# Optimization experiments

Hardware: AMD Instinct MI355X
Metric: run time of the kernel (lower is better)

## Reference

```python
import jax, jax.numpy as jnp
import numpy as np

MARGIN = 0.3
N_GALLERY = 32768
N_BATCH = 1024
D_EMB = 512
N_CLASSES = 1000


def setup_inputs() -> dict:
    key = jax.random.key(0)
    k1, k2, k3, k4 = jax.random.split(key, 4)
    inputs = jax.random.normal(k1, (N_BATCH, D_EMB), dtype=jnp.float32)
    features = jax.random.normal(k2, (N_GALLERY, D_EMB), dtype=jnp.float32)
    feat_labels = jax.random.randint(k3, (N_GALLERY,), 0, N_CLASSES, dtype=jnp.int64 if jax.config.read('jax_enable_x64') else jnp.int32)
    idx = jax.random.randint(k4, (N_BATCH,), 0, N_GALLERY, dtype=feat_labels.dtype)
    # invariant from the original code: idx[i] is in the positive set for targets[i]
    targets = feat_labels[idx]
    return {"inputs": inputs, "features": features, "targets": targets,
            "idx": idx, "feat_labels": feat_labels}


def reference(inputs, features, targets, idx, feat_labels):
    # sim_mat: [n, N] similarity against the gallery bank
    sim = jnp.einsum('nd,Nd->nN', inputs, features)
    n = targets.shape[0]
    # positives: same label in gallery, excluding the sample's own gallery slot
    pos_mask = targets[:, None] == feat_labels[None, :]          # [n, N]
    pos_mask = pos_mask.at[jnp.arange(n), idx].set(False)
    # negatives: every gallery entry with a different label
    neg_mask = targets[:, None] != feat_labels[None, :]          # [n, N]
    pos = jnp.min(jnp.where(pos_mask, sim, jnp.inf), axis=1)     # hardest positive (lowest sim)
    neg = jnp.max(jnp.where(neg_mask, sim, -jnp.inf), axis=1)    # hardest negative (highest sim)
    loss = jnp.maximum(neg - pos + MARGIN, 0.0)
    return jnp.mean(loss)
```

## Files before the change

### kernel.cpp

```cpp
#include <hip/hip_runtime.h>
#include <stdint.h>

#define MARGIN 0.3f
#define M 1024
#define NG 32768
#define K 512
#define BM 256
#define BN 256
#define BK 64
#define KT (K / BK)
#define NTILES (NG / BN)
#define MTILES (M / BM)
#define NPART (NTILES * 4)

typedef __attribute__((ext_vector_type(8))) __bf16 bf16x8;
typedef __attribute__((ext_vector_type(4))) float f32x4;
typedef unsigned short ushort_t;
typedef unsigned int uint_t;

#define BAR() __builtin_amdgcn_s_barrier()
#define LGKM0() asm volatile("s_waitcnt lgkmcnt(0)" ::: "memory")
#define SGB0() __builtin_amdgcn_sched_barrier(0)

static __device__ __forceinline__ ushort_t f2bf(float f) {
    uint_t u = __float_as_uint(f);
    u += 0x7FFFu + ((u >> 16) & 1u);
    return (ushort_t)(u >> 16);
}

__global__ __launch_bounds__(256) void cvt_kernel(const float* __restrict__ src,
                                                  ushort_t* __restrict__ dst, int n8) {
    int i = blockIdx.x * 256 + threadIdx.x;
    if (i >= n8) return;
    const float4* s4 = (const float4*)src;
    float4 a = s4[2 * i];
    float4 b = s4[2 * i + 1];
    uint4 o;
    o.x = (uint_t)f2bf(a.x) | ((uint_t)f2bf(a.y) << 16);
    o.y = (uint_t)f2bf(a.z) | ((uint_t)f2bf(a.w) << 16);
    o.z = (uint_t)f2bf(b.x) | ((uint_t)f2bf(b.y) << 16);
    o.w = (uint_t)f2bf(b.z) | ((uint_t)f2bf(b.w) << 16);
    ((uint4*)dst)[i] = o;
}

static __device__ __forceinline__ void gload_lds16(const void* gptr, void* lptr) {
    __builtin_amdgcn_global_load_lds(
        (const __attribute__((address_space(1))) uint32_t*)(gptr),
        (__attribute__((address_space(3))) uint32_t*)(uintptr_t)(lptr),
        16, 0, 0);
}

static __device__ __forceinline__ bf16x8 lds_read_b128(const ushort_t* p) {
    bf16x8 r;
    asm volatile("ds_read_b128 %0, %1"
                 : "=v"(r)
                 : "v"((const __attribute__((address_space(3))) ushort_t*)p));
    return r;
}

__global__ __launch_bounds__(512, 2) void gemm_kernel(
    const ushort_t* __restrict__ A,
    const ushort_t* __restrict__ B,
    const int* __restrict__ targets,
    const int* __restrict__ idxv,
    const int* __restrict__ labels,
    float* __restrict__ pos_part,
    float* __restrict__ neg_part) {

    __shared__ __align__(16) ushort_t sA[2][BM * BK];
    __shared__ __align__(16) ushort_t sB[2][BN * BK];
    __shared__ int t_s[BM];
    __shared__ int i_s[BM];
    __shared__ int l_s[BN];

    const int tid = threadIdx.x;
    const int lane = tid & 63;
    const int w = tid >> 6;
    const int wm = w >> 2;
    const int wn = w & 3;
    const int l15 = lane & 15;
    const int lhi = lane >> 4;
    const int bid = blockIdx.x;
    const int ntile = bid & (NTILES - 1);
    const int mtile = bid >> 7;

    if (tid < BM) {
        t_s[tid] = targets[mtile * BM + tid];
        i_s[tid] = idxv[mtile * BM + tid];
    } else {
        l_s[tid - BM] = labels[ntile * BN + (tid - BM)];
    }

    f32x4 zero = {0.f, 0.f, 0.f, 0.f};
    f32x4 acc[8][4];
#pragma unroll
    for (int a = 0; a < 8; ++a)
#pragma unroll
        for (int b = 0; b < 4; ++b) acc[a][b] = zero;

    const int rstage = tid >> 3;
    const int cstage = (((tid & 7) ^ (rstage & 7)) << 3);
    const ushort_t* Abase = A + (size_t)mtile * BM * K;
    const ushort_t* Bbase = B + (size_t)ntile * BN * K;

    auto stage_half = [&](const ushort_t* g, ushort_t* l) {
        gload_lds16(g + (size_t)rstage * K + cstage, l + w * 512);
        gload_lds16(g + (size_t)(64 + rstage) * K + cstage, l + 4096 + w * 512);
    };

    auto readA = [&](int buf, int mf, int kk) -> bf16x8 {
        const int r = wm * 128 + mf * 16 + l15;
        const int u = (kk * 4 + lhi) ^ (r & 7);
        return lds_read_b128(&sA[buf][r * 64 + u * 8]);
    };
    auto readB = [&](int buf, int nf, int kk) -> bf16x8 {
        const int r = wn * 64 + nf * 16 + l15;
        const int u = (kk * 4 + lhi) ^ (r & 7);
        return lds_read_b128(&sB[buf][r * 64 + u * 8]);
    };

    stage_half(Abase, &sA[0][0]);
    stage_half(Abase + (size_t)128 * K, &sA[0][8192]);
    stage_half(Bbase, &sB[0][0]);
    stage_half(Bbase + (size_t)128 * K, &sB[0][8192]);
    stage_half(Bbase + BK, &sB[1][0]);
    stage_half(Bbase + BK + (size_t)128 * K, &sB[1][8192]);
    asm volatile("s_waitcnt vmcnt(4)" ::: "memory");
    BAR();

#pragma unroll 1
    for (int kt = 0; kt < KT; ++kt) {
        const int cur = kt & 1;
        bf16x8 av[4], bv[4];

#pragma unroll
        for (int nf = 0; nf < 4; ++nf) bv[nf] = readB(cur, nf, 0);
#pragma unroll
        for (int mf = 0; mf < 4; ++mf) av[mf] = readA(cur, mf, 0);
        if (kt < KT - 1) stage_half(Abase + (size_t)(kt + 1) * BK, &sA[cur ^ 1][0]);
        BAR(); LGKM0(); SGB0();
        __builtin_amdgcn_s_setprio(1);
#pragma unroll
        for (int mf = 0; mf < 4; ++mf)
#pragma unroll
            for (int nf = 0; nf < 4; ++nf)
                acc[mf][nf] = __builtin_amdgcn_mfma_f32_16x16x32_bf16(av[mf], bv[nf], acc[mf][nf], 0, 0, 0);
        __builtin_amdgcn_s_setprio(0);
        BAR();

#pragma unroll
        for (int mf = 0; mf < 4; ++mf) av[mf] = readA(cur, mf + 4, 0);
        if (kt < KT - 1)
            stage_half(Abase + (size_t)(kt + 1) * BK + (size_t)128 * K, &sA[cur ^ 1][8192]);
        BAR(); LGKM0(); SGB0();
        __builtin_amdgcn_s_setprio(1);
#pragma unroll
        for (int mf = 0; mf < 4; ++mf)
#pragma unroll
            for (int nf = 0; nf < 4; ++nf)
                acc[mf + 4][nf] = __builtin_amdgcn_mfma_f32_16x16x32_bf16(av[mf], bv[nf], acc[mf + 4][nf], 0, 0, 0);
        __builtin_amdgcn_s_setprio(0);
        BAR();

#pragma unroll
        for (int nf = 0; nf < 4; ++nf) bv[nf] = readB(cur, nf, 1);
#pragma unroll
        for (int mf = 0; mf < 4; ++mf) av[mf] = readA(cur, mf, 1);
        BAR(); LGKM0(); SGB0();
        __builtin_amdgcn_s_setprio(1);
#pragma unroll
        for (int mf = 0; mf < 4; ++mf)
#pragma unroll
            for (int nf = 0; nf < 4; ++nf)
                acc[mf][nf] = __builtin_amdgcn_mfma_f32_16x16x32_bf16(av[mf], bv[nf], acc[mf][nf], 0, 0, 0);
        __builtin_amdgcn_s_setprio(0);
        BAR();

#pragma unroll
        for (int mf = 0; mf < 4; ++mf) av[mf] = readA(cur, mf + 4, 1);
        if (kt < KT - 2) {
            stage_half(Bbase + (size_t)(kt + 2) * BK, &sB[cur][0]);
            stage_half(Bbase + (size_t)(kt + 2) * BK + (size_t)128 * K, &sB[cur][8192]);
            asm volatile("s_waitcnt vmcnt(4)" ::: "memory");
        } else {
            asm volatile("s_waitcnt vmcnt(0)" ::: "memory");
        }
        BAR(); LGKM0(); SGB0();
        __builtin_amdgcn_s_setprio(1);
#pragma unroll
        for (int mf = 0; mf < 4; ++mf)
#pragma unroll
            for (int nf = 0; nf < 4; ++nf)
                acc[mf + 4][nf] = __builtin_amdgcn_mfma_f32_16x16x32_bf16(av[mf], bv[nf], acc[mf + 4][nf], 0, 0, 0);
        __builtin_amdgcn_s_setprio(0);
        BAR();
    }

    int labv[4], jv[4];
#pragma unroll
    for (int nf = 0; nf < 4; ++nf) {
        const int cl = wn * 64 + nf * 16 + l15;
        labv[nf] = l_s[cl];
        jv[nf] = ntile * BN + cl;
    }
#pragma unroll
    for (int mf = 0; mf < 8; ++mf) {
#pragma unroll
        for (int r = 0; r < 4; ++r) {
            const int row_l = wm * 128 + mf * 16 + lhi * 4 + r;
            const int tgt = t_s[row_l];
            const int exc = i_s[row_l];
            float pmin = INFINITY, nmax = -INFINITY;
#pragma unroll
            for (int nf = 0; nf < 4; ++nf) {
                const float v = acc[mf][nf][r];
                const bool same = (labv[nf] == tgt);
                pmin = fminf(pmin, (same && (jv[nf] != exc)) ? v : INFINITY);
                nmax = fmaxf(nmax, same ? -INFINITY : v);
            }
#pragma unroll
            for (int s = 1; s < 16; s <<= 1) {
                pmin = fminf(pmin, __shfl_xor(pmin, s, 64));
                nmax = fmaxf(nmax, __shfl_xor(nmax, s, 64));
            }
            if (l15 == 0) {
                const int row_g = mtile * BM + row_l;
                pos_part[(size_t)row_g * NPART + ntile * 4 + wn] = pmin;
                neg_part[(size_t)row_g * NPART + ntile * 4 + wn] = nmax;
            }
        }
    }
}

__global__ __launch_bounds__(256) void rowred_kernel(const float* __restrict__ pos_part,
                                                     const float* __restrict__ neg_part,
                                                     float* __restrict__ loss) {
    const int row = blockIdx.x;
    const int t = threadIdx.x;
    const float* pp = pos_part + (size_t)row * NPART;
    const float* nn = neg_part + (size_t)row * NPART;
    float p = fminf(pp[t], pp[t + 256]);
    float nx = fmaxf(nn[t], nn[t + 256]);
#pragma unroll
    for (int s = 1; s < 64; s <<= 1) {
        p = fminf(p, __shfl_xor(p, s, 64));
        nx = fmaxf(nx, __shfl_xor(nx, s, 64));
    }
    __shared__ float sp[4], sn[4];
    if ((t & 63) == 0) { sp[t >> 6] = p; sn[t >> 6] = nx; }
    __syncthreads();
    if (t == 0) {
        p = fminf(fminf(sp[0], sp[1]), fminf(sp[2], sp[3]));
        nx = fmaxf(fmaxf(sn[0], sn[1]), fmaxf(sn[2], sn[3]));
        const float l = nx - p + MARGIN;
        loss[row] = l > 0.f ? l : 0.f;
    }
}

__global__ __launch_bounds__(256) void final_kernel(const float* __restrict__ loss,
                                                    float* __restrict__ out) {
    const int t = threadIdx.x;
    float s = loss[t] + loss[t + 256] + loss[t + 512] + loss[t + 768];
#pragma unroll
    for (int sh = 1; sh < 64; sh <<= 1) s += __shfl_xor(s, sh, 64);
    __shared__ float sb[4];
    if ((t & 63) == 0) sb[t >> 6] = s;
    __syncthreads();
    if (t == 0) out[0] = (sb[0] + sb[1] + sb[2] + sb[3]) * (1.0f / 1024.0f);
}

extern "C" void kernel_launch(void* const* d_in, const int* in_sizes, int n_in,
                              void* d_out, int out_size, void* d_ws, size_t ws_size,
                              hipStream_t stream) {
    const float* inputs = (const float*)d_in[0];
    const float* features = (const float*)d_in[1];
    const int* targets = (const int*)d_in[2];
    const int* idxv = (const int*)d_in[3];
    const int* labels = (const int*)d_in[4];

    char* ws = (char*)d_ws;
    ushort_t* A = (ushort_t*)ws;
    ushort_t* B = (ushort_t*)(ws + (1u << 20));
    float* pos_part = (float*)(ws + (1u << 20) + (32u << 20));
    float* neg_part = pos_part + (size_t)M * NPART;
    float* loss = neg_part + (size_t)M * NPART;

    cvt_kernel<<<(NG * K / 8) / 256, 256, 0, stream>>>(features, B, NG * K / 8);
    cvt_kernel<<<(M * K / 8) / 256, 256, 0, stream>>>(inputs, A, M * K / 8);

    gemm_kernel<<<MTILES * NTILES, 512, 0, stream>>>(A, B, targets, idxv, labels,
                                                     pos_part, neg_part);

    rowred_kernel<<<M, 256, 0, stream>>>(pos_part, neg_part, loss);
    final_kernel<<<1, 256, 0, stream>>>(loss, (float*)d_out);
}
```

Baseline: 163.8 us.

## Restructure GEMM k-loop to one barrier per tile with partial LDS waits

The k-loop now issues all LDS fragment reads for a tile up front, then prefetches the whole next A and B tile into the other buffer. Partial lgkmcnt waits overlap the remaining LDS reads with MFMA groups, and one vmcnt wait plus one barrier per k-tile replaces the many barriers per tile. This cuts synchronisation stalls, but shortens the B prefetch distance from two tiles to one and holds more fragment registers live. Separately, the 16-lane min/max reduction in the epilogue uses DPP moves instead of cross-lane shuffles.

Result: faster. 152.1 us (-7.2%).

```diff
diff --git a/kernel.cpp b/kernel.cpp
--- a/kernel.cpp
+++ b/kernel.cpp
@@ -19,8 +19,9 @@
 typedef unsigned int uint_t;
 
 #define BAR() __builtin_amdgcn_s_barrier()
-#define LGKM0() asm volatile("s_waitcnt lgkmcnt(0)" ::: "memory")
 #define SGB0() __builtin_amdgcn_sched_barrier(0)
+#define WAIT_LGKM(n) asm volatile("s_waitcnt lgkmcnt(" #n ")" ::: "memory")
+#define WAIT_VM0() asm volatile("s_waitcnt vmcnt(0)" ::: "memory")
 
 static __device__ __forceinline__ ushort_t f2bf(float f) {
     uint_t u = __float_as_uint(f);
@@ -58,6 +59,26 @@
     return r;
 }
 
+template <int CTRL>
+static __device__ __forceinline__ float dpp_mv(float x) {
+    return __int_as_float(__builtin_amdgcn_update_dpp(
+        0, __float_as_int(x), CTRL, 0xF, 0xF, true));
+}
+static __device__ __forceinline__ float red16_min(float x) {
+    x = fminf(x, dpp_mv<0xB1>(x));
+    x = fminf(x, dpp_mv<0x4E>(x));
+    x = fminf(x, dpp_mv<0x141>(x));
+    x = fminf(x, dpp_mv<0x140>(x));
+    return x;
+}
+static __device__ __forceinline__ float red16_max(float x) {
+    x = fmaxf(x, dpp_mv<0xB1>(x));
+    x = fmaxf(x, dpp_mv<0x4E>(x));
+    x = fmaxf(x, dpp_mv<0x141>(x));
+    x = fmaxf(x, dpp_mv<0x140>(x));
+    return x;
+}
+
 __global__ __launch_bounds__(512, 2) void gemm_kernel(
     const ushort_t* __restrict__ A,
     const ushort_t* __restrict__ B,
@@ -107,6 +128,12 @@
         gload_lds16(g + (size_t)rstage * K + cstage, l + w * 512);
         gload_lds16(g + (size_t)(64 + rstage) * K + cstage, l + 4096 + w * 512);
     };
+    auto stage_tile = [&](int buf, int kt) {
+        stage_half(Abase + (size_t)kt * BK, &sA[buf][0]);
+        stage_half(Abase + (size_t)kt * BK + (size_t)128 * K, &sA[buf][8192]);
+        stage_half(Bbase + (size_t)kt * BK, &sB[buf][0]);
+        stage_half(Bbase + (size_t)kt * BK + (size_t)128 * K, &sB[buf][8192]);
+    };
 
     auto readA = [&](int buf, int mf, int kk) -> bf16x8 {
         const int r = wm * 128 + mf * 16 + l15;
@@ -119,80 +146,73 @@
         return lds_read_b128(&sB[buf][r * 64 + u * 8]);
     };
 
-    stage_half(Abase, &sA[0][0]);
-    stage_half(Abase + (size_t)128 * K, &sA[0][8192]);
-    stage_half(Bbase, &sB[0][0]);
-    stage_half(Bbase + (size_t)128 * K, &sB[0][8192]);
-    stage_half(Bbase + BK, &sB[1][0]);
-    stage_half(Bbase + BK + (size_t)128 * K, &sB[1][8192]);
-    asm volatile("s_waitcnt vmcnt(4)" ::: "memory");
+    stage_tile(0, 0);
+    WAIT_VM0();
     BAR();
 
 #pragma unroll 1
     for (int kt = 0; kt < KT; ++kt) {
         const int cur = kt & 1;
-        bf16x8 av[4], bv[4];
-
-#pragma unroll
-        for (int nf = 0; nf < 4; ++nf) bv[nf] = readB(cur, nf, 0);
-#pragma unroll
-        for (int mf = 0; mf < 4; ++mf) av[mf] = readA(cur, mf, 0);
-        if (kt < KT - 1) stage_half(Abase + (size_t)(kt + 1) * BK, &sA[cur ^ 1][0]);
-        BAR(); LGKM0(); SGB0();
+        bf16x8 b0[4], a0lo[4], a0hi[4], b1[4], a1lo[4], a1hi[4];
+
+#pragma unroll
+        for (int nf = 0; nf < 4; ++nf) b0[nf] = readB(cur, nf, 0);
+#pragma unroll
+        for (int mf = 0; mf < 4; ++mf) a0lo[mf] = readA(cur, mf, 0);
+#pragma unroll
+        for (int mf = 0; mf < 4; ++mf) a0hi[mf] = readA(cur, mf + 4, 0);
+#pragma unroll
+        for (int nf = 0; nf < 4; ++nf) b1[nf] = readB(cur, nf, 1);
+
+        if (kt + 1 < KT) stage_tile(cur ^ 1, kt + 1);
+
+        WAIT_LGKM(8); SGB0();
         __builtin_amdgcn_s_setprio(1);
 #pragma unroll
         for (int mf = 0; mf < 4; ++mf)
 #pragma unroll
             for (int nf = 0; nf < 4; ++nf)
-                acc[mf][nf] = __builtin_amdgcn_mfma_f32_16x16x32_bf16(av[mf], bv[nf], acc[mf][nf], 0, 0, 0);
+                acc[mf][nf] = __builtin_amdgcn_mfma_f32_16x16x32_bf16(a0lo[mf], b0[nf], acc[mf][nf], 0, 0, 0);
         __builtin_amdgcn_s_setprio(0);
-        BAR();
-
-#pragma unroll
-        for (int mf = 0; mf < 4; ++mf) av[mf] = readA(cur, mf + 4, 0);
-        if (kt < KT - 1)
-            stage_half(Abase + (size_t)(kt + 1) * BK + (size_t)128 * K, &sA[cur ^ 1][8192]);
-        BAR(); LGKM0(); SGB0();
+        SGB0();
+
+#pragma unroll
+        for (int mf = 0; mf < 4; ++mf) a1lo[mf] = readA(cur, mf, 1);
+
+        WAIT_LGKM(8); SGB0();
         __builtin_amdgcn_s_setprio(1);
 #pragma unroll
         for (int mf = 0; mf < 4; ++mf)
 #pragma unroll
             for (int nf = 0; nf < 4; ++nf)
-                acc[mf + 4][nf] = __builtin_amdgcn_mfma_f32_16x16x32_bf16(av[mf], bv[nf], acc[mf + 4][nf], 0, 0, 0);
+                acc[mf + 4][nf] = __builtin_amdgcn_mfma_f32_16x16x32_bf16(a0hi[mf], b0[nf], acc[mf + 4][nf], 0, 0, 0);
         __builtin_amdgcn_s_setprio(0);
-        BAR();
-
-#pragma unroll
-        for (int nf = 0; nf < 4; ++nf) bv[nf] = readB(cur, nf, 1);
-#pragma unroll
-        for (int mf = 0; mf < 4; ++mf) av[mf] = readA(cur, mf, 1);
-        BAR(); LGKM0(); SGB0();
+        SGB0();
+
+#pragma unroll
+        for (int mf = 0; mf < 4; ++mf) a1hi[mf] = readA(cur, mf + 4, 1);
+
+        WAIT_LGKM(4); SGB0();
         __builtin_amdgcn_s_setprio(1);
 #pragma unroll
         for (int mf = 0; mf < 4; ++mf)
 #pragma unroll
             for (int nf = 0; nf < 4; ++nf)
-                acc[mf][nf] = __builtin_amdgcn_mfma_f32_16x16x32_bf16(av[mf], bv[nf], acc[mf][nf], 0, 0, 0);
+                acc[mf][nf] = __builtin_amdgcn_mfma_f32_16x16x32_bf16(a1lo[mf], b1[nf], acc[mf][nf], 0, 0, 0);
         __builtin_amdgcn_s_setprio(0);
-        BAR();
-
-#pragma unroll
-        for (int mf = 0; mf < 4; ++mf) av[mf] = readA(cur, mf + 4, 1);
-        if (kt < KT - 2) {
-            stage_half(Bbase + (size_t)(kt + 2) * BK, &sB[cur][0]);
-            stage_half(Bbase + (size_t)(kt + 2) * BK + (size_t)128 * K, &sB[cur][8192]);
-            asm volatile("s_waitcnt vmcnt(4)" ::: "memory");
-        } else {
-            asm volatile("s_waitcnt vmcnt(0)" ::: "memory");
-        }
-        BAR(); LGKM0(); SGB0();
+        SGB0();
+
+        WAIT_LGKM(0); SGB0();
         __builtin_amdgcn_s_setprio(1);
 #pragma unroll
         for (int mf = 0; mf < 4; ++mf)
 #pragma unroll
             for (int nf = 0; nf < 4; ++nf)
-                acc[mf + 4][nf] = __builtin_amdgcn_mfma_f32_16x16x32_bf16(av[mf], bv[nf], acc[mf + 4][nf], 0, 0, 0);
+                acc[mf + 4][nf] = __builtin_amdgcn_mfma_f32_16x16x32_bf16(a1hi[mf], b1[nf], acc[mf + 4][nf], 0, 0, 0);
         __builtin_amdgcn_s_setprio(0);
+        SGB0();
+
+        WAIT_VM0();
         BAR();
     }
 
@@ -218,11 +238,8 @@
                 pmin = fminf(pmin, (same && (jv[nf] != exc)) ? v : INFINITY);
                 nmax = fmaxf(nmax, same ? -INFINITY : v);
             }
-#pragma unroll
-            for (int s = 1; s < 16; s <<= 1) {
-                pmin = fminf(pmin, __shfl_xor(pmin, s, 64));
-                nmax = fmaxf(nmax, __shfl_xor(nmax, s, 64));
-            }
+            pmin = red16_min(pmin);
+            nmax = red16_max(nmax);
             if (l15 == 0) {
                 const int row_g = mtile * BM + row_l;
                 pos_part[(size_t)row_g * NPART + ntile * 4 + wn] = pmin;
```
